# Kernel optimization log

Hardware: AMD Instinct MI355X
Metric: run time of the kernel (lower is better)

## Reference

```python
import jax, jax.numpy as jnp
import numpy as np

N_NODES = 100000
IN_DIM = 500
HID_DIM = 128
OUT_DIM = 40
N_EDGES = 1600000


def setup_inputs() -> dict:
    key = jax.random.key(0)
    k1, k2, k3, k4, k5 = jax.random.split(key, 5)
    x = jax.random.normal(k1, (N_NODES, IN_DIM), dtype=jnp.float32)
    edge_index = jax.random.randint(k2, (2, N_EDGES), 0, N_NODES, dtype=jnp.int64)
    # Glorot-style init for linear weights, zero bias (as in PyG GCNConv)
    W1 = jax.random.normal(k3, (IN_DIM, HID_DIM), dtype=jnp.float32) / np.sqrt(IN_DIM)
    b1 = jnp.zeros((HID_DIM,), dtype=jnp.float32)
    W2 = jax.random.normal(k4, (HID_DIM, OUT_DIM), dtype=jnp.float32) / np.sqrt(HID_DIM)
    b2 = jnp.zeros((OUT_DIM,), dtype=jnp.float32)
    return {"x": x, "edge_index": edge_index, "W1": W1, "b1": b1, "W2": W2, "b2": b2}


def reference(x, edge_index, W1, b1, W2, b2):
    N = x.shape[0]
    # GCNConv: add self-loops, symmetric normalization deg^-1/2 A deg^-1/2
    loops = jnp.arange(N, dtype=edge_index.dtype)
    src = jnp.concatenate([edge_index[0], loops])  # [E+N]
    dst = jnp.concatenate([edge_index[1], loops])  # [E+N]
    deg = jax.ops.segment_sum(jnp.ones_like(dst, dtype=x.dtype), dst, num_segments=N)
    dinv = jnp.where(deg > 0, jax.lax.rsqrt(deg), 0.0)
    norm = (dinv[src] * dinv[dst])[:, None]  # [E+N, 1]

    def gcn_conv(h, W, b):
        h = h @ W                              # [N, F_out] linear first (PyG order)
        msg = h[src] * norm                    # gather + scale: [E+N, F_out]
        agg = jax.ops.segment_sum(msg, dst, num_segments=N)  # scatter-add
        return agg + b

    h = jax.nn.relu(gcn_conv(x, W1, b1))
    # dropout(p=0.5) is identity in eval mode
    h = gcn_conv(h, W2, b2)
    return jax.nn.log_softmax(h, axis=1)
```

## Files before the change

kernel.cpp:

```cpp
#include <hip/hip_runtime.h>
#include <hip/hip_bf16.h>

#define IN_DIM 500
#define HID 128
#define OUTD 40
#define KPAD 512

typedef __bf16 bf16x8 __attribute__((ext_vector_type(8)));
typedef float f32x16 __attribute__((ext_vector_type(16)));

static __device__ __forceinline__ float rsqrt_acc(float x) {
  float r = rsqrtf(x);
  return r * (1.5f - 0.5f * x * r * r);
}

static __device__ __forceinline__ unsigned short bf16_of(float f) {
  __bf16 h = (__bf16)f;
  return __builtin_bit_cast(unsigned short, h);
}
static __device__ __forceinline__ float bf16_back(unsigned short u) {
  return (float)__builtin_bit_cast(__bf16, u);
}

__global__ void zero_kernel(int* __restrict__ p, int n) {
  int i = blockIdx.x * 256 + threadIdx.x;
  if (i < n) p[i] = 0;
}

__global__ void hist_kernel(const int* __restrict__ dst, int* __restrict__ deg, int E) {
  int e = blockIdx.x * 256 + threadIdx.x;
  if (e < E) atomicAdd(&deg[dst[e]], 1);
}

__global__ void dinv_kernel(const int* __restrict__ deg, float* __restrict__ dinv, int N) {
  int n = blockIdx.x * 256 + threadIdx.x;
  if (n < N) dinv[n] = rsqrt_acc((float)deg[n] + 1.0f);
}

__global__ void scan_a(const int* __restrict__ deg, int* __restrict__ partial,
                       int* __restrict__ blockSums, int N) {
  __shared__ int sums[256];
  int t = threadIdx.x;
  int base = blockIdx.x * 1024 + t * 4;
  int v0 = (base + 0) < N ? deg[base + 0] : 0;
  int v1 = (base + 1) < N ? deg[base + 1] : 0;
  int v2 = (base + 2) < N ? deg[base + 2] : 0;
  int v3 = (base + 3) < N ? deg[base + 3] : 0;
  int l0 = v0, l1 = l0 + v1, l2 = l1 + v2, l3 = l2 + v3;
  sums[t] = l3;
  __syncthreads();
  for (int o = 1; o < 256; o <<= 1) {
    int a = sums[t];
    int b = (t >= o) ? sums[t - o] : 0;
    __syncthreads();
    sums[t] = a + b;
    __syncthreads();
  }
  int excl = sums[t] - l3;
  if (t == 0) blockSums[blockIdx.x] = sums[255];
  if (base + 0 < N) partial[base + 0] = excl;
  if (base + 1 < N) partial[base + 1] = excl + l0;
  if (base + 2 < N) partial[base + 2] = excl + l1;
  if (base + 3 < N) partial[base + 3] = excl + l2;
}

__global__ void scan_b(int* __restrict__ blockSums, int nb) {
  __shared__ int s[256];
  int t = threadIdx.x;
  int orig = (t < nb) ? blockSums[t] : 0;
  s[t] = orig;
  __syncthreads();
  for (int o = 1; o < 256; o <<= 1) {
    int a = s[t];
    int b = (t >= o) ? s[t - o] : 0;
    __syncthreads();
    s[t] = a + b;
    __syncthreads();
  }
  if (t < nb) blockSums[t] = s[t] - orig;
}

__global__ void scan_c(int* __restrict__ row_ptr, const int* __restrict__ blockOff,
                       int* __restrict__ cursor, int N, int E) {
  int n = blockIdx.x * 256 + threadIdx.x;
  if (n < N) {
    int v = row_ptr[n] + blockOff[n >> 10];
    row_ptr[n] = v;
    cursor[n] = v;
  }
  if (n == 0 && blockIdx.x == 0) row_ptr[N] = E;
}

__global__ void place_kernel(const int* __restrict__ src, const int* __restrict__ dst,
                             const float* __restrict__ dinv, int* __restrict__ cursor,
                             int2* __restrict__ ePair, int E) {
  int e = blockIdx.x * 256 + threadIdx.x;
  if (e < E) {
    int s = src[e], d = dst[e];
    int pos = atomicAdd(&cursor[d], 1);
    int2 rec;
    rec.x = s;
    rec.y = __float_as_int(dinv[s] * dinv[d]);
    ePair[pos] = rec;
  }
}

__global__ void convW1_kernel(const float* __restrict__ W1, unsigned short* __restrict__ Whi,
                              unsigned short* __restrict__ Wlo) {
  int idx = blockIdx.x * 256 + threadIdx.x;
  if (idx >= HID * KPAD) return;
  int n = idx >> 9, k = idx & (KPAD - 1);
  float f = (k < IN_DIM) ? W1[(size_t)k * HID + n] : 0.f;
  unsigned short h = bf16_of(f);
  Whi[idx] = h;
  Wlo[idx] = bf16_of(f - bf16_back(h));
}

#define LSTR 40

#define G1_BAR() do { asm volatile("s_waitcnt lgkmcnt(0)" ::: "memory"); \
                      __builtin_amdgcn_s_barrier(); } while (0)

static __device__ __forceinline__ void g1_load(const float* __restrict__ xrow, bool rok,
                                               const unsigned short* __restrict__ Whi,
                                               const unsigned short* __restrict__ Wlo,
                                               int srow, int skoff, int k0,
                                               float (&f)[16], uint4 (&bhv)[2], uint4 (&blv)[2]) {
  if (rok && (k0 + skoff + 16) <= IN_DIM) {
    const float4* p = (const float4*)(xrow + k0 + skoff);
    float4 v0 = p[0], v1 = p[1], v2 = p[2], v3 = p[3];
    f[0]=v0.x; f[1]=v0.y; f[2]=v0.z; f[3]=v0.w;
    f[4]=v1.x; f[5]=v1.y; f[6]=v1.z; f[7]=v1.w;
    f[8]=v2.x; f[9]=v2.y; f[10]=v2.z; f[11]=v2.w;
    f[12]=v3.x; f[13]=v3.y; f[14]=v3.z; f[15]=v3.w;
  } else {
#pragma unroll
    for (int j = 0; j < 16; j++) {
      int k = k0 + skoff + j;
      f[j] = (rok && k < IN_DIM) ? xrow[k] : 0.f;
    }
  }
  const size_t gb = (size_t)srow * KPAD + k0 + skoff;
  bhv[0] = *(const uint4*)&Whi[gb];
  bhv[1] = *(const uint4*)&Whi[gb + 8];
  blv[0] = *(const uint4*)&Wlo[gb];
  blv[1] = *(const uint4*)&Wlo[gb + 8];
}

static __device__ __forceinline__ void g1_stage(unsigned short* sAhi, unsigned short* sAlo,
                                                unsigned short* sBhi, unsigned short* sBlo,
                                                int srow, int skoff, const float (&f)[16],
                                                const uint4 (&bhv)[2], const uint4 (&blv)[2]) {
#pragma unroll
  for (int g = 0; g < 4; g++) {
    ushort4 h, l;
    h.x = bf16_of(f[g*4+0]); l.x = bf16_of(f[g*4+0] - bf16_back(h.x));
    h.y = bf16_of(f[g*4+1]); l.y = bf16_of(f[g*4+1] - bf16_back(h.y));
    h.z = bf16_of(f[g*4+2]); l.z = bf16_of(f[g*4+2] - bf16_back(h.z));
    h.w = bf16_of(f[g*4+3]); l.w = bf16_of(f[g*4+3] - bf16_back(h.w));
    *(ushort4*)&sAhi[srow * LSTR + skoff + g * 4] = h;
    *(ushort4*)&sAlo[srow * LSTR + skoff + g * 4] = l;
  }
  *(uint4*)&sBhi[srow * LSTR + skoff] = bhv[0];
  *(uint4*)&sBhi[srow * LSTR + skoff + 8] = bhv[1];
  *(uint4*)&sBlo[srow * LSTR + skoff] = blv[0];
  *(uint4*)&sBlo[srow * LSTR + skoff + 8] = blv[1];
}

static __device__ __forceinline__ void g1_compute(const unsigned short* sAhi,
                                                  const unsigned short* sAlo,
                                                  const unsigned short* sBhi,
                                                  const unsigned short* sBlo,
                                                  int w, int m, int quad, f32x16 (&acc)[4]) {
#pragma unroll
  for (int sub = 0; sub < 2; sub++) {
    const int ks = sub * 16 + quad * 8;
    bf16x8 ah = *(const bf16x8*)&sAhi[(w * 32 + m) * LSTR + ks];
    bf16x8 al = *(const bf16x8*)&sAlo[(w * 32 + m) * LSTR + ks];
#pragma unroll
    for (int nt = 0; nt < 4; nt++) {
      bf16x8 bh = *(const bf16x8*)&sBhi[(nt * 32 + m) * LSTR + ks];
      bf16x8 bl = *(const bf16x8*)&sBlo[(nt * 32 + m) * LSTR + ks];
      acc[nt] = __builtin_amdgcn_mfma_f32_32x32x16_bf16(ah, bh, acc[nt], 0, 0, 0);
      acc[nt] = __builtin_amdgcn_mfma_f32_32x32x16_bf16(ah, bl, acc[nt], 0, 0, 0);
      acc[nt] = __builtin_amdgcn_mfma_f32_32x32x16_bf16(al, bh, acc[nt], 0, 0, 0);
    }
  }
}

__global__ __launch_bounds__(256) void gemm1_kernel(const float* __restrict__ X,
                                                    const unsigned short* __restrict__ Whi,
                                                    const unsigned short* __restrict__ Wlo,
                                                    float* __restrict__ H1, int N) {
  __shared__ unsigned short sAhi[128 * LSTR];
  __shared__ unsigned short sAlo[128 * LSTR];
  __shared__ unsigned short sBhi[128 * LSTR];
  __shared__ unsigned short sBlo[128 * LSTR];
  const int t = threadIdx.x;
  const int rowBase = blockIdx.x * 128;
  const int lane = t & 63;
  const int w = t >> 6;
  const int m = lane & 31;
  const int quad = lane >> 5;

  f32x16 acc[4];
#pragma unroll
  for (int i = 0; i < 4; i++) acc[i] = (f32x16)(0.f);

  const int srow = t >> 1;
  const int skoff = (t & 1) * 16;
  const bool rok = (rowBase + srow) < N;
  const float* xrow = X + (size_t)(rowBase + (rok ? srow : 0)) * IN_DIM;

  float fA[16]; uint4 bhA[2], blA[2];
  float fB[16]; uint4 bhB[2], blB[2];
  g1_load(xrow, rok, Whi, Wlo, srow, skoff, 0, fA, bhA, blA);

#pragma unroll 1
  for (int r = 0; r < 16; r += 2) {
    g1_stage(sAhi, sAlo, sBhi, sBlo, srow, skoff, fA, bhA, blA);
    G1_BAR();
    g1_load(xrow, rok, Whi, Wlo, srow, skoff, (r + 1) * 32, fB, bhB, blB);
    g1_compute(sAhi, sAlo, sBhi, sBlo, w, m, quad, acc);
    G1_BAR();

    g1_stage(sAhi, sAlo, sBhi, sBlo, srow, skoff, fB, bhB, blB);
    G1_BAR();
    if (r + 2 < 16) g1_load(xrow, rok, Whi, Wlo, srow, skoff, (r + 2) * 32, fA, bhA, blA);
    g1_compute(sAhi, sAlo, sBhi, sBlo, w, m, quad, acc);
    G1_BAR();
  }

#pragma unroll
  for (int nt = 0; nt < 4; nt++) {
#pragma unroll
    for (int r = 0; r < 16; r++) {
      int rowin = (r & 3) + 8 * (r >> 2) + 4 * quad;
      int grow = rowBase + w * 32 + rowin;
      if (grow < N) H1[(size_t)grow * HID + nt * 32 + m] = acc[nt][r];
    }
  }
}

__global__ void agg1_kernel(const float* __restrict__ h1, const int* __restrict__ row_ptr,
                            const int2* __restrict__ ePair, const float* __restrict__ dinv,
                            const float* __restrict__ b1, float* __restrict__ hrelu, int N) {
  int gid = blockIdx.x * 256 + threadIdx.x;
  int n = gid >> 5, c4 = (gid & 31) * 4;
  if (n >= N) return;
  float di = dinv[n];
  float sl = di * di;
  float4 acc = *(const float4*)&h1[(size_t)n * HID + c4];
  acc.x *= sl; acc.y *= sl; acc.z *= sl; acc.w *= sl;
  int i = row_ptr[n];
  const int s1 = row_ptr[n + 1];
  for (; i + 4 <= s1; i += 4) {
    int2 e0 = ePair[i], e1 = ePair[i + 1], e2 = ePair[i + 2], e3 = ePair[i + 3];
    float w0 = __int_as_float(e0.y), w1 = __int_as_float(e1.y);
    float w2 = __int_as_float(e2.y), w3 = __int_as_float(e3.y);
    float4 v0 = *(const float4*)&h1[(size_t)e0.x * HID + c4];
    float4 v1 = *(const float4*)&h1[(size_t)e1.x * HID + c4];
    float4 v2 = *(const float4*)&h1[(size_t)e2.x * HID + c4];
    float4 v3 = *(const float4*)&h1[(size_t)e3.x * HID + c4];
    acc.x += w0 * v0.x + w1 * v1.x + w2 * v2.x + w3 * v3.x;
    acc.y += w0 * v0.y + w1 * v1.y + w2 * v2.y + w3 * v3.y;
    acc.z += w0 * v0.z + w1 * v1.z + w2 * v2.z + w3 * v3.z;
    acc.w += w0 * v0.w + w1 * v1.w + w2 * v2.w + w3 * v3.w;
  }
  for (; i < s1; i++) {
    int2 e = ePair[i];
    float w = __int_as_float(e.y);
    float4 v = *(const float4*)&h1[(size_t)e.x * HID + c4];
    acc.x += w * v.x; acc.y += w * v.y; acc.z += w * v.z; acc.w += w * v.w;
  }
  float4 bb = *(const float4*)&b1[c4];
  float4 r;
  r.x = fmaxf(acc.x + bb.x, 0.f);
  r.y = fmaxf(acc.y + bb.y, 0.f);
  r.z = fmaxf(acc.z + bb.z, 0.f);
  r.w = fmaxf(acc.w + bb.w, 0.f);
  *(float4*)&hrelu[(size_t)n * HID + c4] = r;
}

__global__ __launch_bounds__(256) void gemm2_kernel(const float* __restrict__ A,
                                                    const float* __restrict__ W2,
                                                    float* __restrict__ H2, int N) {
  __shared__ float tA[64 * 129];
  __shared__ float w2s[128 * 48];
  const int t = threadIdx.x;
  const int rowBase = blockIdx.x * 64;
  for (int idx = t; idx < 128 * 48; idx += 256) {
    int k = idx / 48, c = idx - k * 48;
    w2s[idx] = (c < OUTD) ? W2[k * OUTD + c] : 0.f;
  }
  for (int f = t; f < 2048; f += 256) {
    int row = f >> 5, c4 = (f & 31) * 4;
    float4 v = make_float4(0.f, 0.f, 0.f, 0.f);
    if (rowBase + row < N) v = *(const float4*)&A[(size_t)(rowBase + row) * HID + c4];
    tA[row * 129 + c4 + 0] = v.x;
    tA[row * 129 + c4 + 1] = v.y;
    tA[row * 129 + c4 + 2] = v.z;
    tA[row * 129 + c4 + 3] = v.w;
  }
  __syncthreads();
  const int row = t >> 2;
  const int c0 = (t & 3) * 12;
  float acc[12];
#pragma unroll
  for (int j = 0; j < 12; j++) acc[j] = 0.f;
  for (int k = 0; k < HID; k++) {
    float a = tA[row * 129 + k];
    const float* bp = &w2s[k * 48 + c0];
#pragma unroll
    for (int j = 0; j < 12; j++) acc[j] += a * bp[j];
  }
  int r = rowBase + row;
  if (r < N) {
#pragma unroll
    for (int j = 0; j < 12; j++) {
      int c = c0 + j;
      if (c < OUTD) H2[(size_t)r * OUTD + c] = acc[j];
    }
  }
}

__global__ void agg2_kernel(const float* __restrict__ h2, const int* __restrict__ row_ptr,
                            const int2* __restrict__ ePair, const float* __restrict__ dinv,
                            const float* __restrict__ b2, float* __restrict__ out, int N) {
  int gid = blockIdx.x * 256 + threadIdx.x;
  int n = gid / 10;
  int c4 = (gid - n * 10) * 4;
  if (n >= N) return;
  float di = dinv[n];
  float sl = di * di;
  float4 acc = *(const float4*)&h2[(size_t)n * OUTD + c4];
  acc.x *= sl; acc.y *= sl; acc.z *= sl; acc.w *= sl;
  int i = row_ptr[n];
  const int s1 = row_ptr[n + 1];
  for (; i + 4 <= s1; i += 4) {
    int2 e0 = ePair[i], e1 = ePair[i + 1], e2 = ePair[i + 2], e3 = ePair[i + 3];
    float w0 = __int_as_float(e0.y), w1 = __int_as_float(e1.y);
    float w2 = __int_as_float(e2.y), w3 = __int_as_float(e3.y);
    float4 v0 = *(const float4*)&h2[(size_t)e0.x * OUTD + c4];
    float4 v1 = *(const float4*)&h2[(size_t)e1.x * OUTD + c4];
    float4 v2 = *(const float4*)&h2[(size_t)e2.x * OUTD + c4];
    float4 v3 = *(const float4*)&h2[(size_t)e3.x * OUTD + c4];
    acc.x += w0 * v0.x + w1 * v1.x + w2 * v2.x + w3 * v3.x;
    acc.y += w0 * v0.y + w1 * v1.y + w2 * v2.y + w3 * v3.y;
    acc.z += w0 * v0.z + w1 * v1.z + w2 * v2.z + w3 * v3.z;
    acc.w += w0 * v0.w + w1 * v1.w + w2 * v2.w + w3 * v3.w;
  }
  for (; i < s1; i++) {
    int2 e = ePair[i];
    float w = __int_as_float(e.y);
    float4 v = *(const float4*)&h2[(size_t)e.x * OUTD + c4];
    acc.x += w * v.x; acc.y += w * v.y; acc.z += w * v.z; acc.w += w * v.w;
  }
  float* o = &out[(size_t)n * OUTD + c4];
  o[0] = acc.x + b2[c4 + 0];
  o[1] = acc.y + b2[c4 + 1];
  o[2] = acc.z + b2[c4 + 2];
  o[3] = acc.w + b2[c4 + 3];
}

__global__ void lsm_kernel(float* __restrict__ out, int N) {
  int n = blockIdx.x * 256 + threadIdx.x;
  if (n >= N) return;
  float* row = out + (size_t)n * OUTD;
  float v[OUTD];
  float m = -3.4e38f;
#pragma unroll
  for (int j = 0; j < OUTD; j++) {
    v[j] = row[j];
    m = fmaxf(m, v[j]);
  }
  float s = 0.f;
#pragma unroll
  for (int j = 0; j < OUTD; j++) s += expf(v[j] - m);
  float lse = m + logf(s);
#pragma unroll
  for (int j = 0; j < OUTD; j++) row[j] = v[j] - lse;
}

extern "C" void kernel_launch(void* const* d_in, const int* in_sizes, int n_in,
                              void* d_out, int out_size, void* d_ws, size_t ws_size,
                              hipStream_t stream) {
  const float* x  = (const float*)d_in[0];
  const int*   ei = (const int*)d_in[1];
  const float* W1 = (const float*)d_in[2];
  const float* b1 = (const float*)d_in[3];
  const float* W2 = (const float*)d_in[4];
  const float* b2 = (const float*)d_in[5];
  float* out = (float*)d_out;

  const int N = in_sizes[0] / IN_DIM;
  const int E = in_sizes[1] / 2;
  const int* src = ei;
  const int* dst = ei + E;

  char* wsb = (char*)d_ws;
  size_t off = 0;
  auto alloc = [&](size_t bytes) -> char* {
    char* p = wsb + off;
    off = (off + bytes + 1023) & ~(size_t)1023;
    return p;
  };
  int*   deg       = (int*)alloc((size_t)N * 4);
  float* dinv      = (float*)alloc((size_t)N * 4);
  int*   blockSums = (int*)alloc(1024);
  int*   row_ptr   = (int*)alloc((size_t)(N + 1) * 4);
  int*   cursor    = (int*)alloc((size_t)N * 4);
  int2*  ePair     = (int2*)alloc((size_t)E * 8);
  unsigned short* Whi = (unsigned short*)alloc((size_t)HID * KPAD * 2);
  unsigned short* Wlo = (unsigned short*)alloc((size_t)HID * KPAD * 2);
  float* h1        = (float*)alloc((size_t)N * HID * 4);
  float* hrelu     = (float*)alloc((size_t)N * HID * 4);
  float* h2        = h1;
  (void)n_in; (void)out_size;

  if (off > ws_size) return;

  const int gE = (E + 255) / 256;
  const int gN = (N + 255) / 256;
  const int nb = (N + 1023) / 1024;

  zero_kernel<<<gN, 256, 0, stream>>>(deg, N);
  hist_kernel<<<gE, 256, 0, stream>>>(dst, deg, E);
  dinv_kernel<<<gN, 256, 0, stream>>>(deg, dinv, N);
  scan_a<<<nb, 256, 0, stream>>>(deg, row_ptr, blockSums, N);
  scan_b<<<1, 256, 0, stream>>>(blockSums, nb);
  scan_c<<<gN, 256, 0, stream>>>(row_ptr, blockSums, cursor, N, E);
  place_kernel<<<gE, 256, 0, stream>>>(src, dst, dinv, cursor, ePair, E);
  convW1_kernel<<<(HID * KPAD + 255) / 256, 256, 0, stream>>>(W1, Whi, Wlo);

  gemm1_kernel<<<(N + 127) / 128, 256, 0, stream>>>(x, Whi, Wlo, h1, N);
  agg1_kernel<<<(N * 32 + 255) / 256, 256, 0, stream>>>(h1, row_ptr, ePair, dinv, b1, hrelu, N);
  gemm2_kernel<<<(N + 63) / 64, 256, 0, stream>>>(hrelu, W2, h2, N);
  agg2_kernel<<<(N * 10 + 255) / 256, 256, 0, stream>>>(h2, row_ptr, ePair, dinv, b2, out, N);
  lsm_kernel<<<gN, 256, 0, stream>>>(out, N);
}
```

Baseline: 747.3 us.

## Shrink gemm1 row tile to 64 with 2x2 warp layout and single-buffered loads

```diff
diff --git a/kernel.cpp b/kernel.cpp
--- a/kernel.cpp
+++ b/kernel.cpp
@@ -121,123 +121,107 @@
 #define G1_BAR() do { asm volatile("s_waitcnt lgkmcnt(0)" ::: "memory"); \
                       __builtin_amdgcn_s_barrier(); } while (0)
 
-static __device__ __forceinline__ void g1_load(const float* __restrict__ xrow, bool rok,
-                                               const unsigned short* __restrict__ Whi,
-                                               const unsigned short* __restrict__ Wlo,
-                                               int srow, int skoff, int k0,
-                                               float (&f)[16], uint4 (&bhv)[2], uint4 (&blv)[2]) {
-  if (rok && (k0 + skoff + 16) <= IN_DIM) {
-    const float4* p = (const float4*)(xrow + k0 + skoff);
-    float4 v0 = p[0], v1 = p[1], v2 = p[2], v3 = p[3];
-    f[0]=v0.x; f[1]=v0.y; f[2]=v0.z; f[3]=v0.w;
-    f[4]=v1.x; f[5]=v1.y; f[6]=v1.z; f[7]=v1.w;
-    f[8]=v2.x; f[9]=v2.y; f[10]=v2.z; f[11]=v2.w;
-    f[12]=v3.x; f[13]=v3.y; f[14]=v3.z; f[15]=v3.w;
-  } else {
-#pragma unroll
-    for (int j = 0; j < 16; j++) {
-      int k = k0 + skoff + j;
-      f[j] = (rok && k < IN_DIM) ? xrow[k] : 0.f;
-    }
-  }
-  const size_t gb = (size_t)srow * KPAD + k0 + skoff;
-  bhv[0] = *(const uint4*)&Whi[gb];
-  bhv[1] = *(const uint4*)&Whi[gb + 8];
-  blv[0] = *(const uint4*)&Wlo[gb];
-  blv[1] = *(const uint4*)&Wlo[gb + 8];
-}
-
-static __device__ __forceinline__ void g1_stage(unsigned short* sAhi, unsigned short* sAlo,
-                                                unsigned short* sBhi, unsigned short* sBlo,
-                                                int srow, int skoff, const float (&f)[16],
-                                                const uint4 (&bhv)[2], const uint4 (&blv)[2]) {
-#pragma unroll
-  for (int g = 0; g < 4; g++) {
-    ushort4 h, l;
-    h.x = bf16_of(f[g*4+0]); l.x = bf16_of(f[g*4+0] - bf16_back(h.x));
-    h.y = bf16_of(f[g*4+1]); l.y = bf16_of(f[g*4+1] - bf16_back(h.y));
-    h.z = bf16_of(f[g*4+2]); l.z = bf16_of(f[g*4+2] - bf16_back(h.z));
-    h.w = bf16_of(f[g*4+3]); l.w = bf16_of(f[g*4+3] - bf16_back(h.w));
-    *(ushort4*)&sAhi[srow * LSTR + skoff + g * 4] = h;
-    *(ushort4*)&sAlo[srow * LSTR + skoff + g * 4] = l;
-  }
-  *(uint4*)&sBhi[srow * LSTR + skoff] = bhv[0];
-  *(uint4*)&sBhi[srow * LSTR + skoff + 8] = bhv[1];
-  *(uint4*)&sBlo[srow * LSTR + skoff] = blv[0];
-  *(uint4*)&sBlo[srow * LSTR + skoff + 8] = blv[1];
-}
-
-static __device__ __forceinline__ void g1_compute(const unsigned short* sAhi,
-                                                  const unsigned short* sAlo,
-                                                  const unsigned short* sBhi,
-                                                  const unsigned short* sBlo,
-                                                  int w, int m, int quad, f32x16 (&acc)[4]) {
-#pragma unroll
-  for (int sub = 0; sub < 2; sub++) {
-    const int ks = sub * 16 + quad * 8;
-    bf16x8 ah = *(const bf16x8*)&sAhi[(w * 32 + m) * LSTR + ks];
-    bf16x8 al = *(const bf16x8*)&sAlo[(w * 32 + m) * LSTR + ks];
-#pragma unroll
-    for (int nt = 0; nt < 4; nt++) {
-      bf16x8 bh = *(const bf16x8*)&sBhi[(nt * 32 + m) * LSTR + ks];
-      bf16x8 bl = *(const bf16x8*)&sBlo[(nt * 32 + m) * LSTR + ks];
-      acc[nt] = __builtin_amdgcn_mfma_f32_32x32x16_bf16(ah, bh, acc[nt], 0, 0, 0);
-      acc[nt] = __builtin_amdgcn_mfma_f32_32x32x16_bf16(ah, bl, acc[nt], 0, 0, 0);
-      acc[nt] = __builtin_amdgcn_mfma_f32_32x32x16_bf16(al, bh, acc[nt], 0, 0, 0);
-    }
-  }
-}
-
 __global__ __launch_bounds__(256) void gemm1_kernel(const float* __restrict__ X,
                                                     const unsigned short* __restrict__ Whi,
                                                     const unsigned short* __restrict__ Wlo,
                                                     float* __restrict__ H1, int N) {
-  __shared__ unsigned short sAhi[128 * LSTR];
-  __shared__ unsigned short sAlo[128 * LSTR];
+  __shared__ unsigned short sAhi[64 * LSTR];
+  __shared__ unsigned short sAlo[64 * LSTR];
   __shared__ unsigned short sBhi[128 * LSTR];
   __shared__ unsigned short sBlo[128 * LSTR];
   const int t = threadIdx.x;
-  const int rowBase = blockIdx.x * 128;
+  const int rowBase = blockIdx.x * 64;
   const int lane = t & 63;
   const int w = t >> 6;
+  const int rw = w & 1;
+  const int cw = w >> 1;
   const int m = lane & 31;
   const int quad = lane >> 5;
 
-  f32x16 acc[4];
-#pragma unroll
-  for (int i = 0; i < 4; i++) acc[i] = (f32x16)(0.f);
-
-  const int srow = t >> 1;
-  const int skoff = (t & 1) * 16;
-  const bool rok = (rowBase + srow) < N;
-  const float* xrow = X + (size_t)(rowBase + (rok ? srow : 0)) * IN_DIM;
-
-  float fA[16]; uint4 bhA[2], blA[2];
-  float fB[16]; uint4 bhB[2], blB[2];
-  g1_load(xrow, rok, Whi, Wlo, srow, skoff, 0, fA, bhA, blA);
+  f32x16 acc[2];
+  acc[0] = (f32x16)(0.f);
+  acc[1] = (f32x16)(0.f);
+
+  const int arow = t >> 2;
+  const int akoff = (t & 3) * 8;
+  const bool arok = (rowBase + arow) < N;
+  const float* xrow = X + (size_t)(rowBase + (arok ? arow : 0)) * IN_DIM;
+  const int brow = t >> 1;
+  const int bkoff = (t & 1) * 16;
+
+  float f[8];
+  uint4 bh[2], bl[2];
+
+  auto loadA = [&](int k0) {
+    if (arok && (k0 + akoff + 8) <= IN_DIM) {
+      const float4* p = (const float4*)(xrow + k0 + akoff);
+      float4 v0 = p[0], v1 = p[1];
+      f[0] = v0.x; f[1] = v0.y; f[2] = v0.z; f[3] = v0.w;
+      f[4] = v1.x; f[5] = v1.y; f[6] = v1.z; f[7] = v1.w;
+    } else {
+#pragma unroll
+      for (int j = 0; j < 8; j++) {
+        int k = k0 + akoff + j;
+        f[j] = (arok && k < IN_DIM) ? xrow[k] : 0.f;
+      }
+    }
+  };
+  auto loadB = [&](int k0) {
+    const size_t gb = (size_t)brow * KPAD + k0 + bkoff;
+    bh[0] = *(const uint4*)&Whi[gb];
+    bh[1] = *(const uint4*)&Whi[gb + 8];
+    bl[0] = *(const uint4*)&Wlo[gb];
+    bl[1] = *(const uint4*)&Wlo[gb + 8];
+  };
+
+  loadA(0);
+  loadB(0);
 
 #pragma unroll 1
-  for (int r = 0; r < 16; r += 2) {
-    g1_stage(sAhi, sAlo, sBhi, sBlo, srow, skoff, fA, bhA, blA);
+  for (int r = 0; r < 16; r++) {
     G1_BAR();
-    g1_load(xrow, rok, Whi, Wlo, srow, skoff, (r + 1) * 32, fB, bhB, blB);
-    g1_compute(sAhi, sAlo, sBhi, sBlo, w, m, quad, acc);
+#pragma unroll
+    for (int g = 0; g < 2; g++) {
+      ushort4 h, l;
+      h.x = bf16_of(f[g*4+0]); l.x = bf16_of(f[g*4+0] - bf16_back(h.x));
+      h.y = bf16_of(f[g*4+1]); l.y = bf16_of(f[g*4+1] - bf16_back(h.y));
+      h.z = bf16_of(f[g*4+2]); l.z = bf16_of(f[g*4+2] - bf16_back(h.z));
+      h.w = bf16_of(f[g*4+3]); l.w = bf16_of(f[g*4+3] - bf16_back(h.w));
+      *(ushort4*)&sAhi[arow * LSTR + akoff + g * 4] = h;
+      *(ushort4*)&sAlo[arow * LSTR + akoff + g * 4] = l;
+    }
+    *(uint4*)&sBhi[brow * LSTR + bkoff] = bh[0];
+    *(uint4*)&sBhi[brow * LSTR + bkoff + 8] = bh[1];
+    *(uint4*)&sBlo[brow * LSTR + bkoff] = bl[0];
+    *(uint4*)&sBlo[brow * LSTR + bkoff + 8] = bl[1];
+    if (r + 1 < 16) {
+      loadA((r + 1) * 32);
+      loadB((r + 1) * 32);
+    }
     G1_BAR();
-
-    g1_stage(sAhi, sAlo, sBhi, sBlo, srow, skoff, fB, bhB, blB);
-    G1_BAR();
-    if (r + 2 < 16) g1_load(xrow, rok, Whi, Wlo, srow, skoff, (r + 2) * 32, fA, bhA, blA);
-    g1_compute(sAhi, sAlo, sBhi, sBlo, w, m, quad, acc);
-    G1_BAR();
-  }
-
-#pragma unroll
-  for (int nt = 0; nt < 4; nt++) {
+#pragma unroll
+    for (int sub = 0; sub < 2; sub++) {
+      const int ks = sub * 16 + quad * 8;
+      bf16x8 ah = *(const bf16x8*)&sAhi[(rw * 32 + m) * LSTR + ks];
+      bf16x8 al = *(const bf16x8*)&sAlo[(rw * 32 + m) * LSTR + ks];
+#pragma unroll
+      for (int nt = 0; nt < 2; nt++) {
+        bf16x8 bhv = *(const bf16x8*)&sBhi[(cw * 64 + nt * 32 + m) * LSTR + ks];
+        bf16x8 blv = *(const bf16x8*)&sBlo[(cw * 64 + nt * 32 + m) * LSTR + ks];
+        acc[nt] = __builtin_amdgcn_mfma_f32_32x32x16_bf16(ah, bhv, acc[nt], 0, 0, 0);
+        acc[nt] = __builtin_amdgcn_mfma_f32_32x32x16_bf16(ah, blv, acc[nt], 0, 0, 0);
+        acc[nt] = __builtin_amdgcn_mfma_f32_32x32x16_bf16(al, bhv, acc[nt], 0, 0, 0);
+      }
+    }
+  }
+
+#pragma unroll
+  for (int nt = 0; nt < 2; nt++) {
 #pragma unroll
     for (int r = 0; r < 16; r++) {
       int rowin = (r & 3) + 8 * (r >> 2) + 4 * quad;
-      int grow = rowBase + w * 32 + rowin;
-      if (grow < N) H1[(size_t)grow * HID + nt * 32 + m] = acc[nt][r];
+      int grow = rowBase + rw * 32 + rowin;
+      if (grow < N) H1[(size_t)grow * HID + cw * 64 + nt * 32 + m] = acc[nt][r];
     }
   }
 }
@@ -433,7 +417,7 @@
   place_kernel<<<gE, 256, 0, stream>>>(src, dst, dinv, cursor, ePair, E);
   convW1_kernel<<<(HID * KPAD + 255) / 256, 256, 0, stream>>>(W1, Whi, Wlo);
 
-  gemm1_kernel<<<(N + 127) / 128, 256, 0, stream>>>(x, Whi, Wlo, h1, N);
+  gemm1_kernel<<<(N + 63) / 64, 256, 0, stream>>>(x, Whi, Wlo, h1, N);
   agg1_kernel<<<(N * 32 + 255) / 256, 256, 0, stream>>>(h1, row_ptr, ePair, dinv, b1, hrelu, N);
   gemm2_kernel<<<(N + 63) / 64, 256, 0, stream>>>(hrelu, W2, h2, N);
   agg2_kernel<<<(N * 10 + 255) / 256, 256, 0, stream>>>(h2, row_ptr, ePair, dinv, b2, out, N);
```

After: 854.0 us. 14.3% more time.
